# Kernel optimization log

Measured on AMD Instinct MI355X. Metric: run time of the kernel, lower is better.

## Reference

```python
import jax, jax.numpy as jnp
import numpy as np

B, L, D = 8, 4096, 1024   # batch, max words, sent_dim
S, SENT_LEN = 255, 16     # sentences per sample, words per sentence (255*16=4080)
START_BOUND = 1           # leading zero-pad region, as in the torch module


def setup_inputs() -> dict:
    key = jax.random.key(0)
    k1, k2, k3, k4 = jax.random.split(key, 4)
    words_emb = jax.random.normal(k1, (B, L, D), jnp.float32)
    sents_emb = jax.random.normal(k2, (B, S, D), jnp.float32)
    # nn.Linear(2D, D): weight [D, 2D], bias [D]
    W1_w = jax.random.normal(k3, (D, 2 * D), jnp.float32) / np.sqrt(2 * D)
    W1_b = jax.random.normal(k4, (D,), jnp.float32) * 0.01
    # sentence-index-per-word map; -1 marks the zero-padded regions
    sm = -np.ones((B, L), np.int32)
    idx = np.repeat(np.arange(S, dtype=np.int32), SENT_LEN)  # [S*SENT_LEN]
    sm[:, START_BOUND:START_BOUND + S * SENT_LEN] = idx
    sent_map = jnp.asarray(sm)
    return {"words_emb": words_emb, "sents_emb": sents_emb,
            "W1_w": W1_w, "W1_b": W1_b, "sent_map": sent_map}


def reference(words_emb, sents_emb, W1_w, W1_b, sent_map):
    # Expand sentence embeddings to word positions via gather; zero outside spans.
    valid = sent_map >= 0                                    # [B, L]
    safe_idx = jnp.clip(sent_map, 0)                         # [B, L]
    gathered = jnp.take_along_axis(sents_emb, safe_idx[..., None], axis=1)  # [B, L, D]
    sents_state_flat = jnp.where(valid[..., None], gathered, 0.0)
    # concat word + sentence features, then Linear + ReLU
    x = jnp.concatenate([words_emb, sents_state_flat], axis=-1)  # [B, L, 2D]
    return jax.nn.relu(jnp.einsum('ble,de->bld', x, W1_w) + W1_b)
```

## Files before the change

kernel.cpp:

```cpp
#include <hip/hip_runtime.h>
#include <stdint.h>

constexpr int kB = 8;
constexpr int kL = 4096;
constexpr int kD = 1024;
constexpr int kS = 255;
constexpr int kM = kB * kL;
constexpr int kK = 2 * kD;
constexpr int kN = kD;

typedef __bf16 bf16x8 __attribute__((ext_vector_type(8)));
typedef float  f32x4  __attribute__((ext_vector_type(4)));

constexpr size_t WS_WORDS = 0;
constexpr size_t WS_SENTS = WS_WORDS + (size_t)kM * kD * 2;
constexpr size_t WS_W     = WS_SENTS + (size_t)kB * kS * kD * 2;
constexpr size_t WS_ZP    = WS_W + (size_t)kN * kK * 2;
constexpr size_t WS_NEED  = WS_ZP + 3072;

__device__ __forceinline__ uint32_t pk_bf16x2(float a, float b) {
    uint32_t ua = __float_as_uint(a) + 0x8000u;
    uint32_t ub = __float_as_uint(b) + 0x8000u;
    return __builtin_amdgcn_perm(ub, ua, 0x07060302u);
}

__device__ __forceinline__ void async16(const void* g, void* l) {
    __builtin_amdgcn_global_load_lds(
        (const __attribute__((address_space(1))) uint32_t*)g,
        (__attribute__((address_space(3))) uint32_t*)l, 16, 0, 0);
}

#define WAITVM(n)  asm volatile("s_waitcnt vmcnt(" #n ")" ::: "memory")
#define WAITLGKM0  asm volatile("s_waitcnt lgkmcnt(0)" ::: "memory")

__device__ __forceinline__ void blockbar() {
    asm volatile("" ::: "memory");
    __builtin_amdgcn_s_barrier();
    asm volatile("" ::: "memory");
}

__global__ __launch_bounds__(256)
void cvt_prepass2(const float4* __restrict__ words, const float4* __restrict__ sents,
                  const float4* __restrict__ W,
                  uint4* __restrict__ wordsB, uint4* __restrict__ sentsB,
                  uint4* __restrict__ WB, uint32_t* __restrict__ zp)
{
    constexpr size_t NW8 = (size_t)kM * kD / 8;
    constexpr size_t NS8 = (size_t)kB * kS * kD / 8;
    constexpr size_t NB8 = (size_t)kN * kK / 8;
    constexpr size_t NT8 = NW8 + NS8 + NB8;
    if (blockIdx.x == 0) {
        for (int t = threadIdx.x; t < 768; t += 256) zp[t] = 0u;
    }
    const size_t stride = (size_t)gridDim.x * blockDim.x;
    for (size_t i = (size_t)blockIdx.x * blockDim.x + threadIdx.x; i < NT8; i += stride) {
        const float4* src; uint4* dst; size_t j;
        if (i < NW8)            { src = words; dst = wordsB; j = i; }
        else if (i < NW8 + NS8) { src = sents; dst = sentsB; j = i - NW8; }
        else                    { src = W;     dst = WB;     j = i - NW8 - NS8; }
        float4 a  = src[2 * j];
        float4 b2 = src[2 * j + 1];
        uint4 o;
        o.x = pk_bf16x2(a.x,  a.y);
        o.y = pk_bf16x2(a.z,  a.w);
        o.z = pk_bf16x2(b2.x, b2.y);
        o.w = pk_bf16x2(b2.z, b2.w);
        dst[j] = o;
    }
}

__global__ __launch_bounds__(512, 2)
void wsib_gemm_v2(const uint8_t* __restrict__ wordsB,
                  const uint8_t* __restrict__ sentsB,
                  const uint8_t* __restrict__ WB,
                  const float*   __restrict__ bias,
                  const int*     __restrict__ smap,
                  const uint8_t* __restrict__ zp,
                  float* __restrict__ out)
{
    __shared__ uint8_t lds[3][2][16384];

    const int tid  = threadIdx.x;
    const int w    = tid >> 6;
    const int lane = tid & 63;
    const int nT = blockIdx.x;
    const int mT = blockIdx.y;

    const int wm = (w >> 2) * 128;
    const int wn = (w & 3) * 64;
    const int fr = lane & 15, quad = lane >> 4;

    float bv[4];
    #pragma unroll
    for (int ni = 0; ni < 4; ++ni) bv[ni] = bias[nT * 256 + wn + ni * 16 + fr];

    const int lrow = lane >> 2;
    const int cph  = lane & 3;
    const int lc   = cph ^ (lrow & 3) ^ ((lrow >> 2) & 3);
    const int rloc0 = w * 32 + lrow;
    const int rloc1 = rloc0 + 16;
    const int gA0 = mT * 256 + rloc0, gA1 = mT * 256 + rloc1;
    const uint8_t* aw0 = wordsB + (size_t)gA0 * 2048 + lc * 16;
    const uint8_t* aw1 = wordsB + (size_t)gA1 * 2048 + lc * 16;
    const int bIdx = gA0 >> 12;
    const int s0 = smap[gA0], s1 = smap[gA1];
    const uint8_t* as0 = (s0 >= 0) ? sentsB + (size_t)(bIdx * kS + s0) * 2048 + lc * 16
                                   : zp + lc * 16;
    const uint8_t* as1 = (s1 >= 0) ? sentsB + (size_t)(bIdx * kS + s1) * 2048 + lc * 16
                                   : zp + lc * 16;
    const uint8_t* wb0 = WB + (size_t)(nT * 256 + rloc0) * 4096 + lc * 16;
    const uint8_t* wb1 = WB + (size_t)(nT * 256 + rloc1) * 4096 + lc * 16;

    const int pc   = quad ^ (fr & 3) ^ ((fr >> 2) & 3);
    const int offA = (wm + fr) * 64 + pc * 16;
    const int offB = (wn + fr) * 64 + pc * 16;

    f32x4 acc[8][4];
    #pragma unroll
    for (int i = 0; i < 8; ++i)
        #pragma unroll
        for (int j = 0; j < 4; ++j) acc[i][j] = (f32x4){0.f, 0.f, 0.f, 0.f};

    auto srcA0 = [&](int t) { return (t < 32) ? aw0 + (t << 6) : as0 + ((t - 32) << 6); };
    auto srcA1 = [&](int t) { return (t < 32) ? aw1 + (t << 6) : as1 + ((t - 32) << 6); };

    {
        uint8_t* A0 = lds[0][0]; uint8_t* B0 = lds[0][1];
        async16(srcA0(0), A0 + w * 2048);
        async16(srcA1(0), A0 + w * 2048 + 1024);
        async16(wb0,      B0 + w * 2048);
        async16(wb1,      B0 + w * 2048 + 1024);
        uint8_t* A1 = lds[1][0]; uint8_t* B1 = lds[1][1];
        async16(srcA0(1), A1 + w * 2048);
        async16(srcA1(1), A1 + w * 2048 + 1024);
        async16(wb0 + 64, B1 + w * 2048);
        async16(wb1 + 64, B1 + w * 2048 + 1024);
    }

    int bufR = 0;
    #pragma unroll 1
    for (int t = 0; t < 64; ++t) {
        uint8_t* ldsAr = lds[bufR][0];
        uint8_t* ldsBr = lds[bufR][1];
        const int bufS = (bufR == 0) ? 2 : bufR - 1;
        uint8_t* ldsAs = lds[bufS][0];
        uint8_t* ldsBs = lds[bufS][1];
        const int tS = t + 2;

        WAITLGKM0;
        if (t < 63) { WAITVM(4); } else { WAITVM(0); }
        blockbar();

        bf16x8 bf[4];
        #pragma unroll
        for (int ni = 0; ni < 4; ++ni)
            bf[ni] = *(const bf16x8*)(ldsBr + offB + ni * 1024);
        bf16x8 af[4];
        #pragma unroll
        for (int mi = 0; mi < 4; ++mi)
            af[mi] = *(const bf16x8*)(ldsAr + offA + mi * 1024);
        if (tS < 64) {
            async16(srcA0(tS), ldsAs + w * 2048);
            async16(srcA1(tS), ldsAs + w * 2048 + 1024);
        }
        blockbar();
        __builtin_amdgcn_s_setprio(1);
        #pragma unroll
        for (int mi = 0; mi < 4; ++mi)
            #pragma unroll
            for (int ni = 0; ni < 4; ++ni)
                acc[mi][ni] = __builtin_amdgcn_mfma_f32_16x16x32_bf16(
                    af[mi], bf[ni], acc[mi][ni], 0, 0, 0);
        __builtin_amdgcn_s_setprio(0);

        bf16x8 ag[4];
        #pragma unroll
        for (int mi = 0; mi < 4; ++mi)
            ag[mi] = *(const bf16x8*)(ldsAr + offA + (mi + 4) * 1024);
        if (tS < 64) {
            async16(wb0 + (tS << 6), ldsBs + w * 2048);
            async16(wb1 + (tS << 6), ldsBs + w * 2048 + 1024);
        }
        blockbar();
        __builtin_amdgcn_s_setprio(1);
        #pragma unroll
        for (int mi = 0; mi < 4; ++mi)
            #pragma unroll
            for (int ni = 0; ni < 4; ++ni)
                acc[mi + 4][ni] = __builtin_amdgcn_mfma_f32_16x16x32_bf16(
                    ag[mi], bf[ni], acc[mi + 4][ni], 0, 0, 0);
        __builtin_amdgcn_s_setprio(0);

        bufR = (bufR == 2) ? 0 : bufR + 1;
    }

    const int rowBase = mT * 256 + wm + quad * 4;
    const int colBase = nT * 256 + wn + fr;
    #pragma unroll
    for (int mi = 0; mi < 8; ++mi) {
        #pragma unroll
        for (int ni = 0; ni < 4; ++ni) {
            const int col = colBase + ni * 16;
            #pragma unroll
            for (int r = 0; r < 4; ++r) {
                const int row = rowBase + mi * 16 + r;
                out[(size_t)row * kN + col] = fmaxf(acc[mi][ni][r] + bv[ni], 0.f);
            }
        }
    }
}

#define TILE_M 128
#define TILE_N 128
#define TILE_K 32
#define LDS_STRIDE 20
__global__ __launch_bounds__(256)
void wsib_gemm_fb(const float* __restrict__ words, const float* __restrict__ sents,
                  const float* __restrict__ W, const float* __restrict__ bias,
                  const int* __restrict__ smap, float* __restrict__ out)
{
    __shared__ uint32_t Asm[TILE_M * LDS_STRIDE];
    __shared__ uint32_t Bsm[TILE_N * LDS_STRIDE];
    const int tid = threadIdx.x, nT = blockIdx.x, mT = blockIdx.y;
    const int sRow = tid >> 1, half = tid & 1;
    const int mRow = mT * TILE_M + sRow, bIdx = mRow >> 12;
    const float* wsrc = words + (size_t)mRow * kD + half * 16;
    const int sidx = smap[mRow];
    const float* ssrc = (sidx >= 0) ? sents + ((size_t)bIdx * kS + sidx) * kD + half * 16 : nullptr;
    const float* bsrc = W + (size_t)(nT * TILE_N + sRow) * kK + half * 16;
    uint32_t* adst = &Asm[sRow * LDS_STRIDE + half * 8];
    uint32_t* bdst = &Bsm[sRow * LDS_STRIDE + half * 8];
    const int lane = tid & 63, wv = tid >> 6;
    const int wm = (wv & 1) * 64, wn = (wv >> 1) * 64;
    const int fr = lane & 15, quad = lane >> 4;
    f32x4 acc[4][4];
    #pragma unroll
    for (int i = 0; i < 4; ++i)
        #pragma unroll
        for (int j = 0; j < 4; ++j) acc[i][j] = (f32x4){0.f, 0.f, 0.f, 0.f};
    float4 ra[4], rb[4];
    {
        const float4* pa = (const float4*)wsrc; const float4* pb = (const float4*)bsrc;
        #pragma unroll
        for (int i = 0; i < 4; ++i) { ra[i] = pa[i]; rb[i] = pb[i]; }
    }
    for (int k0 = 0; k0 < kK; k0 += TILE_K) {
        uint32_t pa[8], pb[8];
        #pragma unroll
        for (int i = 0; i < 4; ++i) {
            pa[2*i] = pk_bf16x2(ra[i].x, ra[i].y); pa[2*i+1] = pk_bf16x2(ra[i].z, ra[i].w);
            pb[2*i] = pk_bf16x2(rb[i].x, rb[i].y); pb[2*i+1] = pk_bf16x2(rb[i].z, rb[i].w);
        }
        __syncthreads();
        ((uint4*)adst)[0] = make_uint4(pa[0], pa[1], pa[2], pa[3]);
        ((uint4*)adst)[1] = make_uint4(pa[4], pa[5], pa[6], pa[7]);
        ((uint4*)bdst)[0] = make_uint4(pb[0], pb[1], pb[2], pb[3]);
        ((uint4*)bdst)[1] = make_uint4(pb[4], pb[5], pb[6], pb[7]);
        __syncthreads();
        const int k1 = k0 + TILE_K;
        if (k1 < kK) {
            const float* asrc = (k1 < kD) ? (wsrc + k1) : (ssrc ? (ssrc + (k1 - kD)) : nullptr);
            if (asrc) { const float4* p = (const float4*)asrc;
                #pragma unroll
                for (int i = 0; i < 4; ++i) ra[i] = p[i];
            } else {
                #pragma unroll
                for (int i = 0; i < 4; ++i) ra[i] = make_float4(0.f, 0.f, 0.f, 0.f);
            }
            const float4* p = (const float4*)(bsrc + k1);
            #pragma unroll
            for (int i = 0; i < 4; ++i) rb[i] = p[i];
        }
        bf16x8 af[4], bfv[4];
        #pragma unroll
        for (int mi = 0; mi < 4; ++mi)
            af[mi] = *(const bf16x8*)&Asm[(wm + mi * 16 + fr) * LDS_STRIDE + quad * 4];
        #pragma unroll
        for (int ni = 0; ni < 4; ++ni)
            bfv[ni] = *(const bf16x8*)&Bsm[(wn + ni * 16 + fr) * LDS_STRIDE + quad * 4];
        #pragma unroll
        for (int mi = 0; mi < 4; ++mi)
            #pragma unroll
            for (int ni = 0; ni < 4; ++ni)
                acc[mi][ni] = __builtin_amdgcn_mfma_f32_16x16x32_bf16(af[mi], bfv[ni], acc[mi][ni], 0, 0, 0);
    }
    const int rowBase = mT * TILE_M + wm, colBase = nT * TILE_N + wn;
    float bv[4];
    #pragma unroll
    for (int ni = 0; ni < 4; ++ni) bv[ni] = bias[colBase + ni * 16 + fr];
    #pragma unroll
    for (int mi = 0; mi < 4; ++mi)
        #pragma unroll
        for (int ni = 0; ni < 4; ++ni) {
            const int col = colBase + ni * 16 + fr;
            #pragma unroll
            for (int r = 0; r < 4; ++r) {
                const int row = rowBase + mi * 16 + quad * 4 + r;
                out[(size_t)row * kN + col] = fmaxf(acc[mi][ni][r] + bv[ni], 0.f);
            }
        }
}

extern "C" void kernel_launch(void* const* d_in, const int* in_sizes, int n_in,
                              void* d_out, int out_size, void* d_ws, size_t ws_size,
                              hipStream_t stream) {
    const float* words = (const float*)d_in[0];
    const float* sents = (const float*)d_in[1];
    const float* W     = (const float*)d_in[2];
    const float* bias  = (const float*)d_in[3];
    const int*   smap  = (const int*)d_in[4];
    float* out = (float*)d_out;

    if (ws_size >= WS_NEED) {
        uint8_t* ws = (uint8_t*)d_ws;
        uint4* wordsB = (uint4*)(ws + WS_WORDS);
        uint4* sentsB = (uint4*)(ws + WS_SENTS);
        uint4* WB     = (uint4*)(ws + WS_W);
        uint32_t* zp  = (uint32_t*)(ws + WS_ZP);
        cvt_prepass2<<<2048, 256, 0, stream>>>(
            (const float4*)words, (const float4*)sents, (const float4*)W,
            wordsB, sentsB, WB, zp);
        dim3 grid(kN / 256, kM / 256);
        wsib_gemm_v2<<<grid, 512, 0, stream>>>(
            (const uint8_t*)wordsB, (const uint8_t*)sentsB, (const uint8_t*)WB,
            bias, smap, (const uint8_t*)zp, out);
    } else {
        dim3 grid(kN / TILE_N, kM / TILE_M);
        wsib_gemm_fb<<<grid, 256, 0, stream>>>(words, sents, W, bias, smap, out);
    }
}
```

Measured before the change: 373.4 us.

## Fuse fp32-to-bf16 activation conversion into GEMM A-tile loading

Drops the prepass that converted words and sentence embeddings to bf16 in workspace. The GEMM now loads fp32 activations through registers, converts them and writes bf16 into LDS. Only the weight is still converted up front. The main loop also changes: it uses a 4-stage LDS ring with a deeper prefetch, a software-pipelined fragment load for the next k-step, an XCD-aware block swizzle, and sched_barrier in place of asm memory clobbers. This removes a large extra global read/write pass, at the cost of more register pressure and doubled fp32 A-tile traffic inside the GEMM.

Measured after the change: 401.4 us. +7.5%, slower.

```diff
diff --git a/kernel.cpp b/kernel.cpp
--- a/kernel.cpp
+++ b/kernel.cpp
@@ -12,11 +12,9 @@
 typedef __bf16 bf16x8 __attribute__((ext_vector_type(8)));
 typedef float  f32x4  __attribute__((ext_vector_type(4)));
 
-constexpr size_t WS_WORDS = 0;
-constexpr size_t WS_SENTS = WS_WORDS + (size_t)kM * kD * 2;
-constexpr size_t WS_W     = WS_SENTS + (size_t)kB * kS * kD * 2;
-constexpr size_t WS_ZP    = WS_W + (size_t)kN * kK * 2;
-constexpr size_t WS_NEED  = WS_ZP + 3072;
+constexpr size_t WS_W    = 0;
+constexpr size_t WS_ZP   = (size_t)kN * kK * 2;
+constexpr size_t WS_NEED = WS_ZP + 4096;
 
 __device__ __forceinline__ uint32_t pk_bf16x2(float a, float b) {
     uint32_t ua = __float_as_uint(a) + 0x8000u;
@@ -34,57 +32,48 @@
 #define WAITLGKM0  asm volatile("s_waitcnt lgkmcnt(0)" ::: "memory")
 
 __device__ __forceinline__ void blockbar() {
-    asm volatile("" ::: "memory");
+    __builtin_amdgcn_sched_barrier(0);
     __builtin_amdgcn_s_barrier();
-    asm volatile("" ::: "memory");
+    __builtin_amdgcn_sched_barrier(0);
 }
 
 __global__ __launch_bounds__(256)
-void cvt_prepass2(const float4* __restrict__ words, const float4* __restrict__ sents,
-                  const float4* __restrict__ W,
-                  uint4* __restrict__ wordsB, uint4* __restrict__ sentsB,
-                  uint4* __restrict__ WB, uint32_t* __restrict__ zp)
+void cvt_w(const float4* __restrict__ W, uint4* __restrict__ WB,
+           uint32_t* __restrict__ zp)
 {
-    constexpr size_t NW8 = (size_t)kM * kD / 8;
-    constexpr size_t NS8 = (size_t)kB * kS * kD / 8;
-    constexpr size_t NB8 = (size_t)kN * kK / 8;
-    constexpr size_t NT8 = NW8 + NS8 + NB8;
     if (blockIdx.x == 0) {
-        for (int t = threadIdx.x; t < 768; t += 256) zp[t] = 0u;
-    }
-    const size_t stride = (size_t)gridDim.x * blockDim.x;
-    for (size_t i = (size_t)blockIdx.x * blockDim.x + threadIdx.x; i < NT8; i += stride) {
-        const float4* src; uint4* dst; size_t j;
-        if (i < NW8)            { src = words; dst = wordsB; j = i; }
-        else if (i < NW8 + NS8) { src = sents; dst = sentsB; j = i - NW8; }
-        else                    { src = W;     dst = WB;     j = i - NW8 - NS8; }
-        float4 a  = src[2 * j];
-        float4 b2 = src[2 * j + 1];
-        uint4 o;
-        o.x = pk_bf16x2(a.x,  a.y);
-        o.y = pk_bf16x2(a.z,  a.w);
-        o.z = pk_bf16x2(b2.x, b2.y);
-        o.w = pk_bf16x2(b2.z, b2.w);
-        dst[j] = o;
-    }
+        for (int t = threadIdx.x; t < 1024; t += 256) zp[t] = 0u;
+    }
+    size_t i = (size_t)blockIdx.x * 256 + threadIdx.x;
+    float4 a  = W[2 * i];
+    float4 b2 = W[2 * i + 1];
+    uint4 o;
+    o.x = pk_bf16x2(a.x,  a.y);
+    o.y = pk_bf16x2(a.z,  a.w);
+    o.z = pk_bf16x2(b2.x, b2.y);
+    o.w = pk_bf16x2(b2.z, b2.w);
+    WB[i] = o;
 }
 
 __global__ __launch_bounds__(512, 2)
-void wsib_gemm_v2(const uint8_t* __restrict__ wordsB,
-                  const uint8_t* __restrict__ sentsB,
+void wsib_gemm_v3(const float* __restrict__ words,
+                  const float* __restrict__ sents,
                   const uint8_t* __restrict__ WB,
                   const float*   __restrict__ bias,
                   const int*     __restrict__ smap,
-                  const uint8_t* __restrict__ zp,
+                  const float*   __restrict__ zpF,
                   float* __restrict__ out)
 {
-    __shared__ uint8_t lds[3][2][16384];
+    __shared__ uint8_t lds[4][2][16384];
 
     const int tid  = threadIdx.x;
     const int w    = tid >> 6;
     const int lane = tid & 63;
-    const int nT = blockIdx.x;
-    const int mT = blockIdx.y;
+
+    const int lin = blockIdx.y * gridDim.x + blockIdx.x;
+    const int swz = (lin & 7) * 64 + (lin >> 3);
+    const int nT = swz & 3;
+    const int mT = swz >> 2;
 
     const int wm = (w >> 2) * 128;
     const int wn = (w & 3) * 64;
@@ -94,26 +83,24 @@
     #pragma unroll
     for (int ni = 0; ni < 4; ++ni) bv[ni] = bias[nT * 256 + wn + ni * 16 + fr];
 
-    const int lrow = lane >> 2;
-    const int cph  = lane & 3;
-    const int lc   = cph ^ (lrow & 3) ^ ((lrow >> 2) & 3);
-    const int rloc0 = w * 32 + lrow;
-    const int rloc1 = rloc0 + 16;
-    const int gA0 = mT * 256 + rloc0, gA1 = mT * 256 + rloc1;
-    const uint8_t* aw0 = wordsB + (size_t)gA0 * 2048 + lc * 16;
-    const uint8_t* aw1 = wordsB + (size_t)gA1 * 2048 + lc * 16;
-    const int bIdx = gA0 >> 12;
-    const int s0 = smap[gA0], s1 = smap[gA1];
-    const uint8_t* as0 = (s0 >= 0) ? sentsB + (size_t)(bIdx * kS + s0) * 2048 + lc * 16
-                                   : zp + lc * 16;
-    const uint8_t* as1 = (s1 >= 0) ? sentsB + (size_t)(bIdx * kS + s1) * 2048 + lc * 16
-                                   : zp + lc * 16;
-    const uint8_t* wb0 = WB + (size_t)(nT * 256 + rloc0) * 4096 + lc * 16;
-    const uint8_t* wb1 = WB + (size_t)(nT * 256 + rloc1) * 4096 + lc * 16;
-
-    const int pc   = quad ^ (fr & 3) ^ ((fr >> 2) & 3);
-    const int offA = (wm + fr) * 64 + pc * 16;
-    const int offB = (wn + fr) * 64 + pc * 16;
+    const int c = tid & 3;
+    const int gR0 = mT * 256 + (tid >> 2);
+    const int gR1 = gR0 + 128;
+    const float* pW0 = words + (size_t)gR0 * kD + c * 8;
+    const float* pW1 = words + (size_t)gR1 * kD + c * 8;
+    const int bIdx = gR0 >> 12;
+    const int s0 = smap[gR0], s1 = smap[gR1];
+    const float* pS0 = (s0 >= 0) ? sents + (size_t)(bIdx * kS + s0) * kD + c * 8
+                                 : zpF + c * 8;
+    const float* pS1 = (s1 >= 0) ? sents + (size_t)(bIdx * kS + s1) * kD + c * 8
+                                 : zpF + c * 8;
+
+    const int rB0 = w * 32 + (lane >> 2);
+    const uint8_t* pB0 = WB + (size_t)(nT * 256 + rB0) * (kK * 2) + (lane & 3) * 16;
+    const uint8_t* pB1 = pB0 + (size_t)16 * (kK * 2);
+
+    const int offA = (wm + fr) * 64 + quad * 16;
+    const int offB = (wn + fr) * 64 + quad * 16;
 
     f32x4 acc[8][4];
     #pragma unroll
@@ -121,77 +108,102 @@
         #pragma unroll
         for (int j = 0; j < 4; ++j) acc[i][j] = (f32x4){0.f, 0.f, 0.f, 0.f};
 
-    auto srcA0 = [&](int t) { return (t < 32) ? aw0 + (t << 6) : as0 + ((t - 32) << 6); };
-    auto srcA1 = [&](int t) { return (t < 32) ? aw1 + (t << 6) : as1 + ((t - 32) << 6); };
+    auto stageA_load = [&](int t, float4 (&st)[4]) {
+        const float* p0 = (t < 32) ? pW0 + t * 32 : pS0 + (t - 32) * 32;
+        const float* p1 = (t < 32) ? pW1 + t * 32 : pS1 + (t - 32) * 32;
+        st[0] = ((const float4*)p0)[0];
+        st[1] = ((const float4*)p0)[1];
+        st[2] = ((const float4*)p1)[0];
+        st[3] = ((const float4*)p1)[1];
+    };
+    auto stageA_write = [&](uint8_t* bufA, const float4 (&st)[4]) {
+        uint4 o0, o1;
+        o0.x = pk_bf16x2(st[0].x, st[0].y);  o0.y = pk_bf16x2(st[0].z, st[0].w);
+        o0.z = pk_bf16x2(st[1].x, st[1].y);  o0.w = pk_bf16x2(st[1].z, st[1].w);
+        o1.x = pk_bf16x2(st[2].x, st[2].y);  o1.y = pk_bf16x2(st[2].z, st[2].w);
+        o1.z = pk_bf16x2(st[3].x, st[3].y);  o1.w = pk_bf16x2(st[3].z, st[3].w);
+        *(uint4*)(bufA + tid * 16)        = o0;
+        *(uint4*)(bufA + 8192 + tid * 16) = o1;
+    };
+    auto stageB_dma = [&](uint8_t* bufB, int t) {
+        async16(pB0 + t * 64, bufB + w * 2048);
+        async16(pB1 + t * 64, bufB + w * 2048 + 1024);
+    };
 
     {
-        uint8_t* A0 = lds[0][0]; uint8_t* B0 = lds[0][1];
-        async16(srcA0(0), A0 + w * 2048);
-        async16(srcA1(0), A0 + w * 2048 + 1024);
-        async16(wb0,      B0 + w * 2048);
-        async16(wb1,      B0 + w * 2048 + 1024);
-        uint8_t* A1 = lds[1][0]; uint8_t* B1 = lds[1][1];
-        async16(srcA0(1), A1 + w * 2048);
-        async16(srcA1(1), A1 + w * 2048 + 1024);
-        async16(wb0 + 64, B1 + w * 2048);
-        async16(wb1 + 64, B1 + w * 2048 + 1024);
-    }
-
-    int bufR = 0;
-    #pragma unroll 1
-    for (int t = 0; t < 64; ++t) {
-        uint8_t* ldsAr = lds[bufR][0];
-        uint8_t* ldsBr = lds[bufR][1];
-        const int bufS = (bufR == 0) ? 2 : bufR - 1;
-        uint8_t* ldsAs = lds[bufS][0];
-        uint8_t* ldsBs = lds[bufS][1];
-        const int tS = t + 2;
-
-        WAITLGKM0;
-        if (t < 63) { WAITVM(4); } else { WAITVM(0); }
-        blockbar();
-
-        bf16x8 bf[4];
-        #pragma unroll
-        for (int ni = 0; ni < 4; ++ni)
-            bf[ni] = *(const bf16x8*)(ldsBr + offB + ni * 1024);
-        bf16x8 af[4];
-        #pragma unroll
-        for (int mi = 0; mi < 4; ++mi)
-            af[mi] = *(const bf16x8*)(ldsAr + offA + mi * 1024);
-        if (tS < 64) {
-            async16(srcA0(tS), ldsAs + w * 2048);
-            async16(srcA1(tS), ldsAs + w * 2048 + 1024);
-        }
-        blockbar();
+        float4 st[4];
+        #pragma unroll
+        for (int t = 0; t < 3; ++t) {
+            stageA_load(t, st);
+            stageA_write((uint8_t*)lds[t][0], st);
+            stageB_dma((uint8_t*)lds[t][1], t);
+        }
+    }
+    WAITLGKM0;
+    WAITVM(0);
+    blockbar();
+
+    bf16x8 af[4], bfA[4], bfB[4];
+    #pragma unroll
+    for (int mi = 0; mi < 4; ++mi)
+        af[mi] = *(const bf16x8*)((uint8_t*)lds[0][0] + offA + mi * 1024);
+    #pragma unroll
+    for (int ni = 0; ni < 4; ++ni)
+        bfA[ni] = *(const bf16x8*)((uint8_t*)lds[0][1] + offB + ni * 1024);
+
+    auto kstep = [&](int t, bf16x8 (&bfc)[4], bf16x8 (&bfn)[4]) {
+        const int tS = t + 3;
+        uint8_t* bufT  = (uint8_t*)lds[t & 3][0];
+        uint8_t* bufNA = (uint8_t*)lds[(t + 1) & 3][0];
+        uint8_t* bufNB = (uint8_t*)lds[(t + 1) & 3][1];
+        uint8_t* bufSA = (uint8_t*)lds[tS & 3][0];
+        uint8_t* bufSB = (uint8_t*)lds[tS & 3][1];
+
+        float4 st[4];
+        if (tS < 64) stageA_load(tS, st);
+        bf16x8 ag[4];
+        #pragma unroll
+        for (int mi = 0; mi < 4; ++mi)
+            ag[mi] = *(const bf16x8*)(bufT + offA + (mi + 4) * 1024);
         __builtin_amdgcn_s_setprio(1);
         #pragma unroll
         for (int mi = 0; mi < 4; ++mi)
             #pragma unroll
             for (int ni = 0; ni < 4; ++ni)
                 acc[mi][ni] = __builtin_amdgcn_mfma_f32_16x16x32_bf16(
-                    af[mi], bf[ni], acc[mi][ni], 0, 0, 0);
+                    af[mi], bfc[ni], acc[mi][ni], 0, 0, 0);
         __builtin_amdgcn_s_setprio(0);
 
-        bf16x8 ag[4];
-        #pragma unroll
-        for (int mi = 0; mi < 4; ++mi)
-            ag[mi] = *(const bf16x8*)(ldsAr + offA + (mi + 4) * 1024);
+        WAITLGKM0;
+        if (t < 62) { WAITVM(6); } else { WAITVM(0); }
+        blockbar();
+
+        if (t + 1 < 64) {
+            #pragma unroll
+            for (int ni = 0; ni < 4; ++ni)
+                bfn[ni] = *(const bf16x8*)(bufNB + offB + ni * 1024);
+            #pragma unroll
+            for (int mi = 0; mi < 4; ++mi)
+                af[mi] = *(const bf16x8*)(bufNA + offA + mi * 1024);
+        }
         if (tS < 64) {
-            async16(wb0 + (tS << 6), ldsBs + w * 2048);
-            async16(wb1 + (tS << 6), ldsBs + w * 2048 + 1024);
-        }
-        blockbar();
+            stageB_dma(bufSB, tS);
+            stageA_write(bufSA, st);
+        }
         __builtin_amdgcn_s_setprio(1);
         #pragma unroll
         for (int mi = 0; mi < 4; ++mi)
             #pragma unroll
             for (int ni = 0; ni < 4; ++ni)
                 acc[mi + 4][ni] = __builtin_amdgcn_mfma_f32_16x16x32_bf16(
-                    ag[mi], bf[ni], acc[mi + 4][ni], 0, 0, 0);
+                    ag[mi], bfc[ni], acc[mi + 4][ni], 0, 0, 0);
         __builtin_amdgcn_s_setprio(0);
-
-        bufR = (bufR == 2) ? 0 : bufR + 1;
+    };
+
+    #pragma unroll 1
+    for (int t2 = 0; t2 < 32; ++t2) {
+        kstep(2 * t2,     bfA, bfB);
+        kstep(2 * t2 + 1, bfB, bfA);
     }
 
     const int rowBase = mT * 256 + wm + quad * 4;
@@ -313,17 +325,13 @@
 
     if (ws_size >= WS_NEED) {
         uint8_t* ws = (uint8_t*)d_ws;
-        uint4* wordsB = (uint4*)(ws + WS_WORDS);
-        uint4* sentsB = (uint4*)(ws + WS_SENTS);
-        uint4* WB     = (uint4*)(ws + WS_W);
+        uint4* WBv    = (uint4*)(ws + WS_W);
         uint32_t* zp  = (uint32_t*)(ws + WS_ZP);
-        cvt_prepass2<<<2048, 256, 0, stream>>>(
-            (const float4*)words, (const float4*)sents, (const float4*)W,
-            wordsB, sentsB, WB, zp);
+        cvt_w<<<1024, 256, 0, stream>>>((const float4*)W, WBv, zp);
         dim3 grid(kN / 256, kM / 256);
-        wsib_gemm_v2<<<grid, 512, 0, stream>>>(
-            (const uint8_t*)wordsB, (const uint8_t*)sentsB, (const uint8_t*)WB,
-            bias, smap, (const uint8_t*)zp, out);
+        wsib_gemm_v3<<<grid, 512, 0, stream>>>(
+            words, sents, (const uint8_t*)WBv, bias, smap,
+            (const float*)(ws + WS_ZP), out);
     } else {
         dim3 grid(kN / TILE_N, kM / TILE_M);
         wsib_gemm_fb<<<grid, 256, 0, stream>>>(words, sents, W, bias, smap, out);
```

## Deepen GEMM LDS pipeline to four stages with register-prefetched fragments

Applied to the files above, without the earlier changes.

Moves the bf16 GEMM main loop from a 3-buffer LDS ring with two barriers per k-step to a 4-buffer ring with one barrier per k-step. The B and first-half A fragments for the next k-step are loaded into alternating register sets while the current MFMAs run. The goal is to hide LDS read latency and cut barrier stalls. It also drops the XOR swizzle on LDS columns and uses sched_barrier in place of plain compiler fences, which risks LDS bank conflicts and raises LDS use to 128 KB per block.

After: 365.4 us. 2.1% less time.

```diff
diff --git a/kernel.cpp b/kernel.cpp
--- a/kernel.cpp
+++ b/kernel.cpp
@@ -34,9 +34,9 @@
 #define WAITLGKM0  asm volatile("s_waitcnt lgkmcnt(0)" ::: "memory")
 
 __device__ __forceinline__ void blockbar() {
-    asm volatile("" ::: "memory");
+    __builtin_amdgcn_sched_barrier(0);
     __builtin_amdgcn_s_barrier();
-    asm volatile("" ::: "memory");
+    __builtin_amdgcn_sched_barrier(0);
 }
 
 __global__ __launch_bounds__(256)
@@ -70,7 +70,7 @@
 }
 
 __global__ __launch_bounds__(512, 2)
-void wsib_gemm_v2(const uint8_t* __restrict__ wordsB,
+void wsib_gemm_v5(const uint8_t* __restrict__ wordsB,
                   const uint8_t* __restrict__ sentsB,
                   const uint8_t* __restrict__ WB,
                   const float*   __restrict__ bias,
@@ -78,7 +78,7 @@
                   const uint8_t* __restrict__ zp,
                   float* __restrict__ out)
 {
-    __shared__ uint8_t lds[3][2][16384];
+    __shared__ uint8_t lds[4][2][16384];
 
     const int tid  = threadIdx.x;
     const int w    = tid >> 6;
@@ -95,25 +95,31 @@
     for (int ni = 0; ni < 4; ++ni) bv[ni] = bias[nT * 256 + wn + ni * 16 + fr];
 
     const int lrow = lane >> 2;
-    const int cph  = lane & 3;
-    const int lc   = cph ^ (lrow & 3) ^ ((lrow >> 2) & 3);
-    const int rloc0 = w * 32 + lrow;
-    const int rloc1 = rloc0 + 16;
+    const int ch   = (lane & 3) * 16;
+    const int rloc0 = w * 32 + lrow, rloc1 = rloc0 + 16;
     const int gA0 = mT * 256 + rloc0, gA1 = mT * 256 + rloc1;
-    const uint8_t* aw0 = wordsB + (size_t)gA0 * 2048 + lc * 16;
-    const uint8_t* aw1 = wordsB + (size_t)gA1 * 2048 + lc * 16;
     const int bIdx = gA0 >> 12;
+    const uint8_t* aw0 = wordsB + (size_t)gA0 * 2048 + ch;
+    const uint8_t* aw1 = wordsB + (size_t)gA1 * 2048 + ch;
     const int s0 = smap[gA0], s1 = smap[gA1];
-    const uint8_t* as0 = (s0 >= 0) ? sentsB + (size_t)(bIdx * kS + s0) * 2048 + lc * 16
-                                   : zp + lc * 16;
-    const uint8_t* as1 = (s1 >= 0) ? sentsB + (size_t)(bIdx * kS + s1) * 2048 + lc * 16
-                                   : zp + lc * 16;
-    const uint8_t* wb0 = WB + (size_t)(nT * 256 + rloc0) * 4096 + lc * 16;
-    const uint8_t* wb1 = WB + (size_t)(nT * 256 + rloc1) * 4096 + lc * 16;
-
-    const int pc   = quad ^ (fr & 3) ^ ((fr >> 2) & 3);
-    const int offA = (wm + fr) * 64 + pc * 16;
-    const int offB = (wn + fr) * 64 + pc * 16;
+    const uint8_t* as0 = (s0 >= 0) ? sentsB + (size_t)(bIdx * kS + s0) * 2048 + ch : zp + ch;
+    const uint8_t* as1 = (s1 >= 0) ? sentsB + (size_t)(bIdx * kS + s1) * 2048 + ch : zp + ch;
+    const uint8_t* pB0 = WB + (size_t)(nT * 256 + rloc0) * 4096 + ch;
+    const uint8_t* pB1 = WB + (size_t)(nT * 256 + rloc1) * 4096 + ch;
+
+    auto stage = [&](int buf, int t) {
+        uint8_t* A  = (uint8_t*)lds[buf][0];
+        uint8_t* Bb = (uint8_t*)lds[buf][1];
+        const uint8_t* a0 = (t < 32) ? aw0 + t * 64 : as0 + (t - 32) * 64;
+        const uint8_t* a1 = (t < 32) ? aw1 + t * 64 : as1 + (t - 32) * 64;
+        async16(a0, A + w * 2048);
+        async16(a1, A + w * 2048 + 1024);
+        async16(pB0 + t * 64, Bb + w * 2048);
+        async16(pB1 + t * 64, Bb + w * 2048 + 1024);
+    };
+
+    const int offA = (wm + fr) * 64 + quad * 16;
+    const int offB = (wn + fr) * 64 + quad * 16;
 
     f32x4 acc[8][4];
     #pragma unroll
@@ -121,77 +127,65 @@
         #pragma unroll
         for (int j = 0; j < 4; ++j) acc[i][j] = (f32x4){0.f, 0.f, 0.f, 0.f};
 
-    auto srcA0 = [&](int t) { return (t < 32) ? aw0 + (t << 6) : as0 + ((t - 32) << 6); };
-    auto srcA1 = [&](int t) { return (t < 32) ? aw1 + (t << 6) : as1 + ((t - 32) << 6); };
-
-    {
-        uint8_t* A0 = lds[0][0]; uint8_t* B0 = lds[0][1];
-        async16(srcA0(0), A0 + w * 2048);
-        async16(srcA1(0), A0 + w * 2048 + 1024);
-        async16(wb0,      B0 + w * 2048);
-        async16(wb1,      B0 + w * 2048 + 1024);
-        uint8_t* A1 = lds[1][0]; uint8_t* B1 = lds[1][1];
-        async16(srcA0(1), A1 + w * 2048);
-        async16(srcA1(1), A1 + w * 2048 + 1024);
-        async16(wb0 + 64, B1 + w * 2048);
-        async16(wb1 + 64, B1 + w * 2048 + 1024);
-    }
-
-    int bufR = 0;
-    #pragma unroll 1
-    for (int t = 0; t < 64; ++t) {
-        uint8_t* ldsAr = lds[bufR][0];
-        uint8_t* ldsBr = lds[bufR][1];
-        const int bufS = (bufR == 0) ? 2 : bufR - 1;
-        uint8_t* ldsAs = lds[bufS][0];
-        uint8_t* ldsBs = lds[bufS][1];
-        const int tS = t + 2;
-
-        WAITLGKM0;
-        if (t < 63) { WAITVM(4); } else { WAITVM(0); }
-        blockbar();
-
-        bf16x8 bf[4];
-        #pragma unroll
-        for (int ni = 0; ni < 4; ++ni)
-            bf[ni] = *(const bf16x8*)(ldsBr + offB + ni * 1024);
-        bf16x8 af[4];
-        #pragma unroll
-        for (int mi = 0; mi < 4; ++mi)
-            af[mi] = *(const bf16x8*)(ldsAr + offA + mi * 1024);
-        if (tS < 64) {
-            async16(srcA0(tS), ldsAs + w * 2048);
-            async16(srcA1(tS), ldsAs + w * 2048 + 1024);
-        }
-        blockbar();
+    stage(0, 0);
+    stage(1, 1);
+    stage(2, 2);
+    WAITVM(8);
+    blockbar();
+
+    bf16x8 af[4], bfA[4], bfB[4];
+    #pragma unroll
+    for (int mi = 0; mi < 4; ++mi)
+        af[mi] = *(const bf16x8*)((uint8_t*)lds[0][0] + offA + mi * 1024);
+    #pragma unroll
+    for (int ni = 0; ni < 4; ++ni)
+        bfA[ni] = *(const bf16x8*)((uint8_t*)lds[0][1] + offB + ni * 1024);
+
+    auto kstep = [&](int t, bf16x8 (&bfc)[4], bf16x8 (&bfn)[4]) {
+        uint8_t* bufT = (uint8_t*)lds[t & 3][0];
+
+        bf16x8 ag[4];
+        #pragma unroll
+        for (int mi = 0; mi < 4; ++mi)
+            ag[mi] = *(const bf16x8*)(bufT + offA + (mi + 4) * 1024);
         __builtin_amdgcn_s_setprio(1);
         #pragma unroll
         for (int mi = 0; mi < 4; ++mi)
             #pragma unroll
             for (int ni = 0; ni < 4; ++ni)
                 acc[mi][ni] = __builtin_amdgcn_mfma_f32_16x16x32_bf16(
-                    af[mi], bf[ni], acc[mi][ni], 0, 0, 0);
+                    af[mi], bfc[ni], acc[mi][ni], 0, 0, 0);
         __builtin_amdgcn_s_setprio(0);
 
-        bf16x8 ag[4];
-        #pragma unroll
-        for (int mi = 0; mi < 4; ++mi)
-            ag[mi] = *(const bf16x8*)(ldsAr + offA + (mi + 4) * 1024);
-        if (tS < 64) {
-            async16(wb0 + (tS << 6), ldsBs + w * 2048);
-            async16(wb1 + (tS << 6), ldsBs + w * 2048 + 1024);
-        }
+        WAITLGKM0;
+        if (t < 62) { WAITVM(4); } else { WAITVM(0); }
         blockbar();
+
+        if (t + 3 < 64) stage((t + 3) & 3, t + 3);
+        if (t + 1 < 64) {
+            uint8_t* bufNA = (uint8_t*)lds[(t + 1) & 3][0];
+            uint8_t* bufNB = (uint8_t*)lds[(t + 1) & 3][1];
+            #pragma unroll
+            for (int ni = 0; ni < 4; ++ni)
+                bfn[ni] = *(const bf16x8*)(bufNB + offB + ni * 1024);
+            #pragma unroll
+            for (int mi = 0; mi < 4; ++mi)
+                af[mi] = *(const bf16x8*)(bufNA + offA + mi * 1024);
+        }
         __builtin_amdgcn_s_setprio(1);
         #pragma unroll
         for (int mi = 0; mi < 4; ++mi)
             #pragma unroll
             for (int ni = 0; ni < 4; ++ni)
                 acc[mi + 4][ni] = __builtin_amdgcn_mfma_f32_16x16x32_bf16(
-                    ag[mi], bf[ni], acc[mi + 4][ni], 0, 0, 0);
+                    ag[mi], bfc[ni], acc[mi + 4][ni], 0, 0, 0);
         __builtin_amdgcn_s_setprio(0);
-
-        bufR = (bufR == 2) ? 0 : bufR + 1;
+    };
+
+    #pragma unroll 1
+    for (int t2 = 0; t2 < 32; ++t2) {
+        kstep(2 * t2,     bfA, bfB);
+        kstep(2 * t2 + 1, bfB, bfA);
     }
 
     const int rowBase = mT * 256 + wm + quad * 4;
@@ -321,7 +315,7 @@
             (const float4*)words, (const float4*)sents, (const float4*)W,
             wordsB, sentsB, WB, zp);
         dim3 grid(kN / 256, kM / 256);
-        wsib_gemm_v2<<<grid, 512, 0, stream>>>(
+        wsib_gemm_v5<<<grid, 512, 0, stream>>>(
             (const uint8_t*)wordsB, (const uint8_t*)sentsB, (const uint8_t*)WB,
             bias, smap, (const uint8_t*)zp, out);
     } else {
```
